# Kernel optimization log

Measured on AMD Instinct MI355X. Metric: run time of the kernel, lower is better.

Reference implementation:

```python
import jax, jax.numpy as jnp
import numpy as np


def _unpack_i4(packed):
    """Unpack int8 bytes into two signed int4 values (low nibble first),
    matching quarot.functional.pack_i4's interleaved layout."""
    p = packed.astype(jnp.int8)
    low = jnp.right_shift(jnp.left_shift(p, 4), 4)   # sign-extended low nibble
    high = jnp.right_shift(p, 4)                      # arithmetic shift -> signed high nibble
    return jnp.stack([low, high], axis=-1).reshape(*p.shape[:-1], p.shape[-1] * 2)


def setup_inputs() -> dict:
    key = jax.random.key(0)
    k1, k2, k3, k4 = jax.random.split(key, 4)
    M, K, N = 4096, 4096, 11008
    # packed int4 activations / weights: each byte holds two signed 4-bit values
    x_q = jax.random.randint(k1, (M, K // 2), 0, 256, dtype=jnp.int32)
    weight = jax.random.randint(k3, (N, K // 2), 0, 256, dtype=jnp.int32)
    # per-row dequant scales (small positive values, as real quant scales are)
    scales_x = (jax.random.uniform(k2, (M, 1), dtype=jnp.float32) * 0.01 + 1e-3).astype(jnp.float16)
    weight_scales = (jax.random.uniform(k4, (N,), dtype=jnp.float32) * 0.01 + 1e-3).astype(jnp.float16)
    return {"x_q": x_q, "scales_x": scales_x, "weight": weight, "weight_scales": weight_scales}


def reference(x_q, scales_x, weight, weight_scales):
    # Unpack int4 -> exact small integers; fp32 matmul accumulates them exactly
    # (|sum| <= 8*8*4096 < 2^24), emulating quarot.fuse_matmul's int4 GEMM.
    A = _unpack_i4(x_q).astype(jnp.float32)      # [M, K]
    B = _unpack_i4(weight).astype(jnp.float32)   # [N, K]
    acc = jnp.einsum('mk,nk->mn', A, B)          # [M, N] integer-exact GEMM
    # fused per-row (activation) x per-channel (weight) dequantization
    out = acc * scales_x.astype(jnp.float32) * weight_scales.astype(jnp.float32)[None, :]
    return out.astype(jnp.float16)
```

## Files before the change

### kernel.cpp

```cpp
#include <hip/hip_runtime.h>

typedef int v4i __attribute__((ext_vector_type(4)));

#define M_DIM 4096
#define N_DIM 11008
#define K_DIM 4096
#define KP    (K_DIM / 2)
#define NKT   (K_DIM / 64)

__device__ __forceinline__ unsigned pack2(int p) {
    int lo = (p << 28) >> 28;
    int hi = (p << 24) >> 28;
    return (unsigned)(lo & 0xFF) | ((unsigned)(hi & 0xFF) << 8);
}

__device__ __forceinline__ void unpack_group(int4 p, unsigned &slo, unsigned &shi) {
    unsigned c = ((unsigned)p.x & 0xFFu)
               | (((unsigned)p.y & 0xFFu) << 8)
               | (((unsigned)p.z & 0xFFu) << 16)
               | (((unsigned)p.w & 0xFFu) << 24);
    slo = (c & 0x0F0F0F0Fu) | ((c & 0x08080808u) * 30u);
    unsigned d = c >> 4;
    shi = (d & 0x0F0F0F0Fu) | ((d & 0x08080808u) * 30u);
}

__global__ __launch_bounds__(256) void unpack_i4_all(
    const int* __restrict__ inA, const int* __restrict__ inB,
    uint2* __restrict__ out, int n4A, int n4tot)
{
    for (int idx = blockIdx.x * blockDim.x + threadIdx.x; idx < n4tot;
         idx += gridDim.x * blockDim.x) {
        int4 v;
        if (idx < n4A) v = ((const int4*)inA)[idx];
        else           v = ((const int4*)inB)[idx - n4A];
        unsigned d0 = pack2(v.x) | (pack2(v.y) << 16);
        unsigned d1 = pack2(v.z) | (pack2(v.w) << 16);
        out[idx] = make_uint2(d0, d1);
    }
}

__global__ __launch_bounds__(512, 2) void gemm_i8_kernel(
    const unsigned char* __restrict__ A8, const unsigned char* __restrict__ B8,
    const float* __restrict__ sx, const float* __restrict__ sw,
    float* __restrict__ out)
{
    __shared__ v4i smem[8192];
    unsigned char* smemAll = (unsigned char*)smem;

    const int t    = threadIdx.x;
    const int lane = t & 63;
    const int w    = t >> 6;
    const int wm   = w >> 2;
    const int wn   = w & 3;

    const int orig = blockIdx.x;
    const int wgid = (orig & 7) * 86 + (orig >> 3);
    const int bx   = wgid >> 4;
    const int by   = wgid & 15;
    const int rowBase = by * 256;
    const int colBase = bx * 256;

    const int cA0 = t, cA1 = t + 512;
    const int rA0 = (cA0 >> 6) * 16 + (cA0 & 15);
    const int rA1 = (cA1 >> 6) * 16 + (cA1 & 15);
    const int qA0 = ((cA0 >> 4) & 3) * 16;
    const int qA1 = ((cA1 >> 4) & 3) * 16;

    const unsigned char* gA0 = A8 + (size_t)(rowBase + rA0) * K_DIM + qA0;
    const unsigned char* gA1 = A8 + (size_t)(rowBase + rA1) * K_DIM + qA1;
    const unsigned char* gB0 = B8 + (size_t)(colBase + rA0) * K_DIM + qA0;
    const unsigned char* gB1 = B8 + (size_t)(colBase + rA1) * K_DIM + qA1;

    const int oA0 = cA0 * 16;
    const int oA1 = cA1 * 16;
    const int oB0 = 16384 + cA0 * 16;
    const int oB1 = 16384 + cA1 * 16;

    v4i acc[8][4] = {};

#define STAGE_A(S) do {                                                        \
    unsigned char* _sb = smemAll + (((S) & 3) << 15);                          \
    const int _kb = (S) * 64;                                                  \
    __builtin_amdgcn_global_load_lds(                                          \
        (const __attribute__((address_space(1))) void*)(gA0 + _kb),            \
        (__attribute__((address_space(3))) void*)(_sb + oA0), 16, 0, 0);       \
    __builtin_amdgcn_global_load_lds(                                          \
        (const __attribute__((address_space(1))) void*)(gA1 + _kb),            \
        (__attribute__((address_space(3))) void*)(_sb + oA1), 16, 0, 0);       \
} while (0)

#define STAGE_B(S) do {                                                        \
    unsigned char* _sb = smemAll + (((S) & 3) << 15);                          \
    const int _kb = (S) * 64;                                                  \
    __builtin_amdgcn_global_load_lds(                                          \
        (const __attribute__((address_space(1))) void*)(gB0 + _kb),            \
        (__attribute__((address_space(3))) void*)(_sb + oB0), 16, 0, 0);       \
    __builtin_amdgcn_global_load_lds(                                          \
        (const __attribute__((address_space(1))) void*)(gB1 + _kb),            \
        (__attribute__((address_space(3))) void*)(_sb + oB1), 16, 0, 0);       \
} while (0)

#define COMPUTE_PHASED(S, DO_STAGE, SS) do {                                   \
    const unsigned char* _b = smemAll + (((S) & 3) << 15);                     \
    v4i bf[4], af0[4], af1[4];                                                 \
     \
    _Pragma("unroll")                                                          \
    for (int nt = 0; nt < 4; ++nt)                                             \
        bf[nt] = *((const v4i*)(_b + 16384 + (((wn * 4 + nt) * 64 + lane) << 4))); \
    _Pragma("unroll")                                                          \
    for (int mt = 0; mt < 4; ++mt)                                             \
        af0[mt] = *((const v4i*)(_b + (((wm * 8 + mt) * 64 + lane) << 4)));    \
    if (DO_STAGE) STAGE_A(SS);                                                 \
    __builtin_amdgcn_s_barrier();                                              \
    asm volatile("s_waitcnt lgkmcnt(0)" ::: "memory");                         \
    __builtin_amdgcn_sched_barrier(0);                                         \
    __builtin_amdgcn_s_setprio(1);                                             \
    _Pragma("unroll")                                                          \
    for (int mt = 0; mt < 4; ++mt)                                             \
        _Pragma("unroll")                                                      \
        for (int nt = 0; nt < 4; ++nt)                                         \
            acc[mt][nt] = __builtin_amdgcn_mfma_i32_16x16x64_i8(               \
                af0[mt], bf[nt], acc[mt][nt], 0, 0, 0);                        \
    __builtin_amdgcn_s_setprio(0);                                             \
    __builtin_amdgcn_s_barrier();                                              \
    __builtin_amdgcn_sched_barrier(0);                                         \
     \
    _Pragma("unroll")                                                          \
    for (int mt = 0; mt < 4; ++mt)                                             \
        af1[mt] = *((const v4i*)(_b + (((wm * 8 + 4 + mt) * 64 + lane) << 4))); \
    if (DO_STAGE) STAGE_B(SS);                                                 \
    __builtin_amdgcn_s_barrier();                                              \
    asm volatile("s_waitcnt lgkmcnt(0)" ::: "memory");                         \
    __builtin_amdgcn_sched_barrier(0);                                         \
    __builtin_amdgcn_s_setprio(1);                                             \
    _Pragma("unroll")                                                          \
    for (int mt = 0; mt < 4; ++mt)                                             \
        _Pragma("unroll")                                                      \
        for (int nt = 0; nt < 4; ++nt)                                         \
            acc[4 + mt][nt] = __builtin_amdgcn_mfma_i32_16x16x64_i8(           \
                af1[mt], bf[nt], acc[4 + mt][nt], 0, 0, 0);                    \
    __builtin_amdgcn_s_setprio(0);                                             \
} while (0)

    STAGE_A(0); STAGE_B(0);
    STAGE_A(1); STAGE_B(1);
    STAGE_A(2); STAGE_B(2);

    for (int kt = 0; kt < NKT - 3; ++kt) {
        asm volatile("s_waitcnt vmcnt(8)" ::: "memory");
        __builtin_amdgcn_s_barrier();
        __builtin_amdgcn_sched_barrier(0);
        COMPUTE_PHASED(kt, 1, kt + 3);
    }
    asm volatile("s_waitcnt vmcnt(8)" ::: "memory");
    __builtin_amdgcn_s_barrier();
    __builtin_amdgcn_sched_barrier(0);
    COMPUTE_PHASED(NKT - 3, 0, 0);
    asm volatile("s_waitcnt vmcnt(4)" ::: "memory");
    __builtin_amdgcn_s_barrier();
    __builtin_amdgcn_sched_barrier(0);
    COMPUTE_PHASED(NKT - 2, 0, 0);
    asm volatile("s_waitcnt vmcnt(0)" ::: "memory");
    __builtin_amdgcn_s_barrier();
    __builtin_amdgcn_sched_barrier(0);
    COMPUTE_PHASED(NKT - 1, 0, 0);

#undef STAGE_A
#undef STAGE_B
#undef COMPUTE_PHASED

    const int ccol = lane & 15;
    const int crow = (lane >> 4) * 4;

    float xs[8][4];
    #pragma unroll
    for (int mt = 0; mt < 8; ++mt)
        #pragma unroll
        for (int r = 0; r < 4; ++r)
            xs[mt][r] = sx[rowBase + wm * 128 + mt * 16 + crow + r];

    #pragma unroll
    for (int nt = 0; nt < 4; ++nt) {
        const int gn = colBase + wn * 64 + nt * 16 + ccol;
        const float wsc = sw[gn];
        #pragma unroll
        for (int mt = 0; mt < 8; ++mt) {
            const int gm = rowBase + wm * 128 + mt * 16 + crow;
            #pragma unroll
            for (int r = 0; r < 4; ++r) {
                float v = (float)acc[mt][nt][r] * xs[mt][r] * wsc;
                out[(size_t)(gm + r) * N_DIM + gn] = v;
            }
        }
    }
}

__global__ __launch_bounds__(256) void gemm_i4_fused_kernel(
    const int* __restrict__ Aq, const int* __restrict__ Bq,
    const float* __restrict__ sx, const float* __restrict__ sw,
    float* __restrict__ out)
{
    __shared__ v4i smem[1024];
    unsigned char* smemA = (unsigned char*)smem;
    unsigned char* smemB = smemA + 8192;

    const int t    = threadIdx.x;
    const int lane = t & 63;
    const int w    = t >> 6;
    const int wm   = w >> 1;
    const int wn   = w & 1;
    const int rowBase = blockIdx.y * 128;
    const int colBase = blockIdx.x * 128;

    const int c0 = t, c1 = t + 256;
    const int r0 = (c0 >> 6) * 16 + (c0 & 15);
    const int r1 = (c1 >> 6) * 16 + (c1 & 15);
    const int q0 = (c0 >> 4) & 3;
    const int q1 = (c1 >> 4) & 3;

    const int* gA0 = Aq + (size_t)(rowBase + r0) * KP + q0 * 8;
    const int* gA1 = Aq + (size_t)(rowBase + r1) * KP + q1 * 8;
    const int* gB0 = Bq + (size_t)(colBase + r0) * KP + q0 * 8;
    const int* gB1 = Bq + (size_t)(colBase + r1) * KP + q1 * 8;

    v4i* lA0 = (v4i*)(smemA + c0 * 16);
    v4i* lA1 = (v4i*)(smemA + c1 * 16);
    v4i* lB0 = (v4i*)(smemB + c0 * 16);
    v4i* lB1 = (v4i*)(smemB + c1 * 16);

    v4i acc[4][4] = {};

    for (int kb = 0; kb < K_DIM; kb += 64) {
        const int kp = kb >> 1;
        int4 a00 = *(const int4*)(gA0 + kp);
        int4 a01 = *(const int4*)(gA0 + kp + 4);
        int4 a10 = *(const int4*)(gA1 + kp);
        int4 a11 = *(const int4*)(gA1 + kp + 4);
        int4 b00 = *(const int4*)(gB0 + kp);
        int4 b01 = *(const int4*)(gB0 + kp + 4);
        int4 b10 = *(const int4*)(gB1 + kp);
        int4 b11 = *(const int4*)(gB1 + kp + 4);

        __syncthreads();

        unsigned u0, u1, u2, u3;
        unpack_group(a00, u0, u1); unpack_group(a01, u2, u3);
        *lA0 = (v4i){(int)u0, (int)u1, (int)u2, (int)u3};
        unpack_group(a10, u0, u1); unpack_group(a11, u2, u3);
        *lA1 = (v4i){(int)u0, (int)u1, (int)u2, (int)u3};
        unpack_group(b00, u0, u1); unpack_group(b01, u2, u3);
        *lB0 = (v4i){(int)u0, (int)u1, (int)u2, (int)u3};
        unpack_group(b10, u0, u1); unpack_group(b11, u2, u3);
        *lB1 = (v4i){(int)u0, (int)u1, (int)u2, (int)u3};

        __syncthreads();

        v4i af[4], bf[4];
        #pragma unroll
        for (int mt = 0; mt < 4; ++mt)
            af[mt] = *((const v4i*)(smemA + ((wm * 4 + mt) * 64 + lane) * 16));
        #pragma unroll
        for (int nt = 0; nt < 4; ++nt)
            bf[nt] = *((const v4i*)(smemB + ((wn * 4 + nt) * 64 + lane) * 16));

        #pragma unroll
        for (int mt = 0; mt < 4; ++mt)
            #pragma unroll
            for (int nt = 0; nt < 4; ++nt)
                acc[mt][nt] = __builtin_amdgcn_mfma_i32_16x16x64_i8(
                    af[mt], bf[nt], acc[mt][nt], 0, 0, 0);
    }

    const int ccol = lane & 15;
    const int crow = (lane >> 4) * 4;

    float xs[4][4];
    #pragma unroll
    for (int mt = 0; mt < 4; ++mt)
        #pragma unroll
        for (int r = 0; r < 4; ++r)
            xs[mt][r] = sx[rowBase + wm * 64 + mt * 16 + crow + r];

    #pragma unroll
    for (int nt = 0; nt < 4; ++nt) {
        const int gn = colBase + wn * 64 + nt * 16 + ccol;
        const float wsc = sw[gn];
        #pragma unroll
        for (int mt = 0; mt < 4; ++mt) {
            const int gm = rowBase + wm * 64 + mt * 16 + crow;
            #pragma unroll
            for (int r = 0; r < 4; ++r) {
                float v = (float)acc[mt][nt][r] * xs[mt][r] * wsc;
                out[(size_t)(gm + r) * N_DIM + gn] = v;
            }
        }
    }
}

extern "C" void kernel_launch(void* const* d_in, const int* in_sizes, int n_in,
                              void* d_out, int out_size, void* d_ws, size_t ws_size,
                              hipStream_t stream) {
    (void)in_sizes; (void)n_in; (void)out_size;
    const int*   x_q = (const int*)d_in[0];
    const float* sx  = (const float*)d_in[1];
    const int*   w_q = (const int*)d_in[2];
    const float* sw  = (const float*)d_in[3];
    float*       out = (float*)d_out;

    const size_t needA = (size_t)M_DIM * K_DIM;
    const size_t needB = (size_t)N_DIM * K_DIM;
    if (ws_size >= needA + needB) {
        unsigned char* A8 = (unsigned char*)d_ws;
        unsigned char* B8 = A8 + needA;
        const int n4A = M_DIM * KP / 4;
        const int n4B = N_DIM * KP / 4;
        const int n4T = n4A + n4B;
        unpack_i4_all<<<2048, 256, 0, stream>>>(x_q, w_q, (uint2*)d_ws, n4A, n4T);
        gemm_i8_kernel<<<688, 512, 0, stream>>>(A8, B8, sx, sw, out);
    } else {
        dim3 grid(N_DIM / 128, M_DIM / 128);
        gemm_i4_fused_kernel<<<grid, 256, 0, stream>>>(x_q, w_q, sx, sw, out);
    }
}
```

Baseline: 484.1 us.

## Double-buffer register fragments so LDS reads overlap MFMAs of previous k-tile

Replaces the two-phase per-k-tile compute, which had barriers between the A halves, with a software-pipelined loop. Each iteration issues inline-asm ds_read_b128 loads for the next tile's A/B fragments into one register set while the MFMAs run on the other set, and it uses a single barrier per iteration. Staging of A and B global->LDS loads is merged into one macro. This removes the extra barrier and LDS read latency on the critical path, at the cost of doubling fragment registers (24 extra v4i), which may hurt occupancy or cause spills. Wait counts and buffer reuse with a 4-slot ring must remain correct.

After: 491.1 us. About the same (+1.5%).

```diff
diff --git a/kernel.cpp b/kernel.cpp
--- a/kernel.cpp
+++ b/kernel.cpp
@@ -76,9 +76,15 @@
     const int oB0 = 16384 + cA0 * 16;
     const int oB1 = 16384 + cA1 * 16;
 
+    const unsigned ldsBase =
+        (unsigned)(size_t)(__attribute__((address_space(3))) void*)smemAll;
+    const unsigned aAddrBase = ldsBase + (unsigned)(wm * 8192 + lane * 16);
+    const unsigned bAddrBase = ldsBase + (unsigned)(16384 + wn * 4096 + lane * 16);
+
     v4i acc[8][4] = {};
-
-#define STAGE_A(S) do {                                                        \
+    v4i aFA[8], bFA[4], aFB[8], bFB[4];
+
+#define STAGE_AB(S) do {                                                       \
     unsigned char* _sb = smemAll + (((S) & 3) << 15);                          \
     const int _kb = (S) * 64;                                                  \
     __builtin_amdgcn_global_load_lds(                                          \
@@ -87,11 +93,6 @@
     __builtin_amdgcn_global_load_lds(                                          \
         (const __attribute__((address_space(1))) void*)(gA1 + _kb),            \
         (__attribute__((address_space(3))) void*)(_sb + oA1), 16, 0, 0);       \
-} while (0)
-
-#define STAGE_B(S) do {                                                        \
-    unsigned char* _sb = smemAll + (((S) & 3) << 15);                          \
-    const int _kb = (S) * 64;                                                  \
     __builtin_amdgcn_global_load_lds(                                          \
         (const __attribute__((address_space(1))) void*)(gB0 + _kb),            \
         (__attribute__((address_space(3))) void*)(_sb + oB0), 16, 0, 0);       \
@@ -100,74 +101,67 @@
         (__attribute__((address_space(3))) void*)(_sb + oB1), 16, 0, 0);       \
 } while (0)
 
-#define COMPUTE_PHASED(S, DO_STAGE, SS) do {                                   \
-    const unsigned char* _b = smemAll + (((S) & 3) << 15);                     \
-    v4i bf[4], af0[4], af1[4];                                                 \
-     \
-    _Pragma("unroll")                                                          \
-    for (int nt = 0; nt < 4; ++nt)                                             \
-        bf[nt] = *((const v4i*)(_b + 16384 + (((wn * 4 + nt) * 64 + lane) << 4))); \
-    _Pragma("unroll")                                                          \
-    for (int mt = 0; mt < 4; ++mt)                                             \
-        af0[mt] = *((const v4i*)(_b + (((wm * 8 + mt) * 64 + lane) << 4)));    \
-    if (DO_STAGE) STAGE_A(SS);                                                 \
-    __builtin_amdgcn_s_barrier();                                              \
-    asm volatile("s_waitcnt lgkmcnt(0)" ::: "memory");                         \
-    __builtin_amdgcn_sched_barrier(0);                                         \
+#define READ_FRAGS(AS, BS, KT) do {                                            \
+    const unsigned _bo = ((unsigned)(KT) & 3u) << 15;                          \
+    unsigned _aAddr = aAddrBase + _bo;                                         \
+    unsigned _bAddr = bAddrBase + _bo;                                         \
+    asm volatile("ds_read_b128 %0, %1 offset:0"    : "=v"(BS[0]) : "v"(_bAddr)); \
+    asm volatile("ds_read_b128 %0, %1 offset:1024" : "=v"(BS[1]) : "v"(_bAddr)); \
+    asm volatile("ds_read_b128 %0, %1 offset:2048" : "=v"(BS[2]) : "v"(_bAddr)); \
+    asm volatile("ds_read_b128 %0, %1 offset:3072" : "=v"(BS[3]) : "v"(_bAddr)); \
+    asm volatile("ds_read_b128 %0, %1 offset:0"    : "=v"(AS[0]) : "v"(_aAddr)); \
+    asm volatile("ds_read_b128 %0, %1 offset:1024" : "=v"(AS[1]) : "v"(_aAddr)); \
+    asm volatile("ds_read_b128 %0, %1 offset:2048" : "=v"(AS[2]) : "v"(_aAddr)); \
+    asm volatile("ds_read_b128 %0, %1 offset:3072" : "=v"(AS[3]) : "v"(_aAddr)); \
+    asm volatile("ds_read_b128 %0, %1 offset:4096" : "=v"(AS[4]) : "v"(_aAddr)); \
+    asm volatile("ds_read_b128 %0, %1 offset:5120" : "=v"(AS[5]) : "v"(_aAddr)); \
+    asm volatile("ds_read_b128 %0, %1 offset:6144" : "=v"(AS[6]) : "v"(_aAddr)); \
+    asm volatile("ds_read_b128 %0, %1 offset:7168" : "=v"(AS[7]) : "v"(_aAddr)); \
+} while (0)
+
+#define MFMA_ALL(AS, BS) do {                                                  \
     __builtin_amdgcn_s_setprio(1);                                             \
     _Pragma("unroll")                                                          \
-    for (int mt = 0; mt < 4; ++mt)                                             \
+    for (int mt = 0; mt < 8; ++mt)                                             \
         _Pragma("unroll")                                                      \
         for (int nt = 0; nt < 4; ++nt)                                         \
             acc[mt][nt] = __builtin_amdgcn_mfma_i32_16x16x64_i8(               \
-                af0[mt], bf[nt], acc[mt][nt], 0, 0, 0);                        \
-    __builtin_amdgcn_s_setprio(0);                                             \
-    __builtin_amdgcn_s_barrier();                                              \
-    __builtin_amdgcn_sched_barrier(0);                                         \
-     \
-    _Pragma("unroll")                                                          \
-    for (int mt = 0; mt < 4; ++mt)                                             \
-        af1[mt] = *((const v4i*)(_b + (((wm * 8 + 4 + mt) * 64 + lane) << 4))); \
-    if (DO_STAGE) STAGE_B(SS);                                                 \
-    __builtin_amdgcn_s_barrier();                                              \
-    asm volatile("s_waitcnt lgkmcnt(0)" ::: "memory");                         \
-    __builtin_amdgcn_sched_barrier(0);                                         \
-    __builtin_amdgcn_s_setprio(1);                                             \
-    _Pragma("unroll")                                                          \
-    for (int mt = 0; mt < 4; ++mt)                                             \
-        _Pragma("unroll")                                                      \
-        for (int nt = 0; nt < 4; ++nt)                                         \
-            acc[4 + mt][nt] = __builtin_amdgcn_mfma_i32_16x16x64_i8(           \
-                af1[mt], bf[nt], acc[4 + mt][nt], 0, 0, 0);                    \
+                AS[mt], BS[nt], acc[mt][nt], 0, 0, 0);                         \
     __builtin_amdgcn_s_setprio(0);                                             \
 } while (0)
 
-    STAGE_A(0); STAGE_B(0);
-    STAGE_A(1); STAGE_B(1);
-    STAGE_A(2); STAGE_B(2);
-
-    for (int kt = 0; kt < NKT - 3; ++kt) {
-        asm volatile("s_waitcnt vmcnt(8)" ::: "memory");
-        __builtin_amdgcn_s_barrier();
-        __builtin_amdgcn_sched_barrier(0);
-        COMPUTE_PHASED(kt, 1, kt + 3);
-    }
+#define KITER(RA, RB, MA, MB, KT, VMC, DO_STAGE) do {                          \
+    asm volatile("s_waitcnt vmcnt(" #VMC ") lgkmcnt(0)" ::: "memory");         \
+    __builtin_amdgcn_sched_barrier(0);                                         \
+    __builtin_amdgcn_s_barrier();                                              \
+    READ_FRAGS(RA, RB, KT);                                                    \
+    if (DO_STAGE) STAGE_AB((KT) + 3);                                          \
+    __builtin_amdgcn_sched_barrier(0);                                         \
+    MFMA_ALL(MA, MB);                                                          \
+} while (0)
+
+    STAGE_AB(0); STAGE_AB(1); STAGE_AB(2);
     asm volatile("s_waitcnt vmcnt(8)" ::: "memory");
     __builtin_amdgcn_s_barrier();
+    READ_FRAGS(aFA, bFA, 0);
+    STAGE_AB(3);
     __builtin_amdgcn_sched_barrier(0);
-    COMPUTE_PHASED(NKT - 3, 0, 0);
-    asm volatile("s_waitcnt vmcnt(4)" ::: "memory");
-    __builtin_amdgcn_s_barrier();
+
+    for (int kt = 1; kt <= 59; kt += 2) {
+        KITER(aFB, bFB, aFA, bFA, kt,     8, 1);
+        KITER(aFA, bFA, aFB, bFB, kt + 1, 8, 1);
+    }
+    KITER(aFB, bFB, aFA, bFA, 61, 8, 0);
+    KITER(aFA, bFA, aFB, bFB, 62, 4, 0);
+    KITER(aFB, bFB, aFA, bFA, 63, 0, 0);
+    asm volatile("s_waitcnt lgkmcnt(0)" ::: "memory");
     __builtin_amdgcn_sched_barrier(0);
-    COMPUTE_PHASED(NKT - 2, 0, 0);
-    asm volatile("s_waitcnt vmcnt(0)" ::: "memory");
-    __builtin_amdgcn_s_barrier();
-    __builtin_amdgcn_sched_barrier(0);
-    COMPUTE_PHASED(NKT - 1, 0, 0);
-
-#undef STAGE_A
-#undef STAGE_B
-#undef COMPUTE_PHASED
+    MFMA_ALL(aFB, bFB);
+
+#undef STAGE_AB
+#undef READ_FRAGS
+#undef MFMA_ALL
+#undef KITER
 
     const int ccol = lane & 15;
     const int crow = (lane >> 4) * 4;
```

## Keep operands as packed int4 in workspace and unpack in registers before MFMA

Applied to the files above, without the earlier changes.

The preprocessing pass now packs the int32-per-byte inputs into dense int4 bytes instead of expanding them to int8, halving its output size and the workspace. The GEMM stages packed tiles covering K=128 into LDS and sign-extends nibbles in registers into two int8 fragments per load, then issues two i8 MFMAs per fragment pair. This halves global and LDS traffic per K step and cuts the barrier count per tile by dropping the two-phase A/B staging. In exchange it adds VALU unpack work inside the MFMA loop, which could compete with matrix issue and raise register pressure.

New measurement: 497.1 us. +2.7%, slower.

```diff
diff --git a/kernel.cpp b/kernel.cpp
--- a/kernel.cpp
+++ b/kernel.cpp
@@ -6,7 +6,8 @@
 #define N_DIM 11008
 #define K_DIM 4096
 #define KP    (K_DIM / 2)
-#define NKT   (K_DIM / 64)
+#define KPB   (K_DIM / 2)
+#define NKT2  (K_DIM / 128)
 
 __device__ __forceinline__ unsigned pack2(int p) {
     int lo = (p << 28) >> 28;
@@ -24,23 +25,37 @@
     shi = (d & 0x0F0F0F0Fu) | ((d & 0x08080808u) * 30u);
 }
 
-__global__ __launch_bounds__(256) void unpack_i4_all(
+__device__ __forceinline__ int sx4(unsigned u) {
+    unsigned a = u & 0x0F0F0F0Fu;
+    unsigned s = u & 0x08080808u;
+    return (int)(a | ((s << 5) - (s << 1)));
+}
+
+__device__ __forceinline__ void unpack16(v4i r, v4i &f0, v4i &f1) {
+    unsigned w0 = (unsigned)r[0], w1 = (unsigned)r[1];
+    unsigned w2 = (unsigned)r[2], w3 = (unsigned)r[3];
+    f0[0] = sx4(w0); f0[1] = sx4(w0 >> 4); f0[2] = sx4(w1); f0[3] = sx4(w1 >> 4);
+    f1[0] = sx4(w2); f1[1] = sx4(w2 >> 4); f1[2] = sx4(w3); f1[3] = sx4(w3 >> 4);
+}
+
+__global__ __launch_bounds__(256) void pack_i4_all(
     const int* __restrict__ inA, const int* __restrict__ inB,
-    uint2* __restrict__ out, int n4A, int n4tot)
+    unsigned* __restrict__ out, int n4A, int n4tot)
 {
     for (int idx = blockIdx.x * blockDim.x + threadIdx.x; idx < n4tot;
          idx += gridDim.x * blockDim.x) {
         int4 v;
         if (idx < n4A) v = ((const int4*)inA)[idx];
         else           v = ((const int4*)inB)[idx - n4A];
-        unsigned d0 = pack2(v.x) | (pack2(v.y) << 16);
-        unsigned d1 = pack2(v.z) | (pack2(v.w) << 16);
-        out[idx] = make_uint2(d0, d1);
-    }
-}
-
-__global__ __launch_bounds__(512, 2) void gemm_i8_kernel(
-    const unsigned char* __restrict__ A8, const unsigned char* __restrict__ B8,
+        out[idx] = ((unsigned)v.x & 0xFFu)
+                 | (((unsigned)v.y & 0xFFu) << 8)
+                 | (((unsigned)v.z & 0xFFu) << 16)
+                 | (((unsigned)v.w & 0xFFu) << 24);
+    }
+}
+
+__global__ __launch_bounds__(512, 2) void gemm_i4p_kernel(
+    const unsigned char* __restrict__ A4, const unsigned char* __restrict__ B4,
     const float* __restrict__ sx, const float* __restrict__ sw,
     float* __restrict__ out)
 {
@@ -66,10 +81,10 @@
     const int qA0 = ((cA0 >> 4) & 3) * 16;
     const int qA1 = ((cA1 >> 4) & 3) * 16;
 
-    const unsigned char* gA0 = A8 + (size_t)(rowBase + rA0) * K_DIM + qA0;
-    const unsigned char* gA1 = A8 + (size_t)(rowBase + rA1) * K_DIM + qA1;
-    const unsigned char* gB0 = B8 + (size_t)(colBase + rA0) * K_DIM + qA0;
-    const unsigned char* gB1 = B8 + (size_t)(colBase + rA1) * K_DIM + qA1;
+    const unsigned char* gA0 = A4 + (size_t)(rowBase + rA0) * KPB + qA0;
+    const unsigned char* gA1 = A4 + (size_t)(rowBase + rA1) * KPB + qA1;
+    const unsigned char* gB0 = B4 + (size_t)(colBase + rA0) * KPB + qA0;
+    const unsigned char* gB1 = B4 + (size_t)(colBase + rA1) * KPB + qA1;
 
     const int oA0 = cA0 * 16;
     const int oA1 = cA1 * 16;
@@ -78,7 +93,7 @@
 
     v4i acc[8][4] = {};
 
-#define STAGE_A(S) do {                                                        \
+#define STAGE_AB(S) do {                                                       \
     unsigned char* _sb = smemAll + (((S) & 3) << 15);                          \
     const int _kb = (S) * 64;                                                  \
     __builtin_amdgcn_global_load_lds(                                          \
@@ -87,11 +102,6 @@
     __builtin_amdgcn_global_load_lds(                                          \
         (const __attribute__((address_space(1))) void*)(gA1 + _kb),            \
         (__attribute__((address_space(3))) void*)(_sb + oA1), 16, 0, 0);       \
-} while (0)
-
-#define STAGE_B(S) do {                                                        \
-    unsigned char* _sb = smemAll + (((S) & 3) << 15);                          \
-    const int _kb = (S) * 64;                                                  \
     __builtin_amdgcn_global_load_lds(                                          \
         (const __attribute__((address_space(1))) void*)(gB0 + _kb),            \
         (__attribute__((address_space(3))) void*)(_sb + oB0), 16, 0, 0);       \
@@ -100,74 +110,58 @@
         (__attribute__((address_space(3))) void*)(_sb + oB1), 16, 0, 0);       \
 } while (0)
 
-#define COMPUTE_PHASED(S, DO_STAGE, SS) do {                                   \
-    const unsigned char* _b = smemAll + (((S) & 3) << 15);                     \
-    v4i bf[4], af0[4], af1[4];                                                 \
-     \
+#define TILE(KT, DO_STAGE) do {                                                \
+    const unsigned char* _b = smemAll + (((KT) & 3) << 15);                    \
+    v4i braw[4], araw[8];                                                      \
     _Pragma("unroll")                                                          \
     for (int nt = 0; nt < 4; ++nt)                                             \
-        bf[nt] = *((const v4i*)(_b + 16384 + (((wn * 4 + nt) * 64 + lane) << 4))); \
+        braw[nt] = *((const v4i*)(_b + 16384 + (((wn * 4 + nt) * 64 + lane) << 4))); \
     _Pragma("unroll")                                                          \
-    for (int mt = 0; mt < 4; ++mt)                                             \
-        af0[mt] = *((const v4i*)(_b + (((wm * 8 + mt) * 64 + lane) << 4)));    \
-    if (DO_STAGE) STAGE_A(SS);                                                 \
-    __builtin_amdgcn_s_barrier();                                              \
-    asm volatile("s_waitcnt lgkmcnt(0)" ::: "memory");                         \
-    __builtin_amdgcn_sched_barrier(0);                                         \
-    __builtin_amdgcn_s_setprio(1);                                             \
+    for (int mt = 0; mt < 8; ++mt)                                             \
+        araw[mt] = *((const v4i*)(_b + (((wm * 8 + mt) * 64 + lane) << 4)));   \
+    if (DO_STAGE) STAGE_AB((KT) + 3);                                          \
+    v4i bf0[4], bf1[4];                                                        \
     _Pragma("unroll")                                                          \
-    for (int mt = 0; mt < 4; ++mt)                                             \
+    for (int nt = 0; nt < 4; ++nt) unpack16(braw[nt], bf0[nt], bf1[nt]);       \
+    _Pragma("unroll")                                                          \
+    for (int mt = 0; mt < 8; ++mt) {                                           \
+        v4i a0, a1;                                                            \
+        unpack16(araw[mt], a0, a1);                                            \
+        __builtin_amdgcn_s_setprio(1);                                         \
         _Pragma("unroll")                                                      \
-        for (int nt = 0; nt < 4; ++nt)                                         \
+        for (int nt = 0; nt < 4; ++nt) {                                       \
             acc[mt][nt] = __builtin_amdgcn_mfma_i32_16x16x64_i8(               \
-                af0[mt], bf[nt], acc[mt][nt], 0, 0, 0);                        \
-    __builtin_amdgcn_s_setprio(0);                                             \
-    __builtin_amdgcn_s_barrier();                                              \
-    __builtin_amdgcn_sched_barrier(0);                                         \
-     \
-    _Pragma("unroll")                                                          \
-    for (int mt = 0; mt < 4; ++mt)                                             \
-        af1[mt] = *((const v4i*)(_b + (((wm * 8 + 4 + mt) * 64 + lane) << 4))); \
-    if (DO_STAGE) STAGE_B(SS);                                                 \
-    __builtin_amdgcn_s_barrier();                                              \
-    asm volatile("s_waitcnt lgkmcnt(0)" ::: "memory");                         \
-    __builtin_amdgcn_sched_barrier(0);                                         \
-    __builtin_amdgcn_s_setprio(1);                                             \
-    _Pragma("unroll")                                                          \
-    for (int mt = 0; mt < 4; ++mt)                                             \
-        _Pragma("unroll")                                                      \
-        for (int nt = 0; nt < 4; ++nt)                                         \
-            acc[4 + mt][nt] = __builtin_amdgcn_mfma_i32_16x16x64_i8(           \
-                af1[mt], bf[nt], acc[4 + mt][nt], 0, 0, 0);                    \
-    __builtin_amdgcn_s_setprio(0);                                             \
+                a0, bf0[nt], acc[mt][nt], 0, 0, 0);                            \
+            acc[mt][nt] = __builtin_amdgcn_mfma_i32_16x16x64_i8(               \
+                a1, bf1[nt], acc[mt][nt], 0, 0, 0);                            \
+        }                                                                      \
+        __builtin_amdgcn_s_setprio(0);                                         \
+    }                                                                          \
 } while (0)
 
-    STAGE_A(0); STAGE_B(0);
-    STAGE_A(1); STAGE_B(1);
-    STAGE_A(2); STAGE_B(2);
-
-    for (int kt = 0; kt < NKT - 3; ++kt) {
+    STAGE_AB(0); STAGE_AB(1); STAGE_AB(2);
+
+    for (int kt = 0; kt < NKT2 - 3; ++kt) {
         asm volatile("s_waitcnt vmcnt(8)" ::: "memory");
         __builtin_amdgcn_s_barrier();
         __builtin_amdgcn_sched_barrier(0);
-        COMPUTE_PHASED(kt, 1, kt + 3);
+        TILE(kt, 1);
     }
     asm volatile("s_waitcnt vmcnt(8)" ::: "memory");
     __builtin_amdgcn_s_barrier();
     __builtin_amdgcn_sched_barrier(0);
-    COMPUTE_PHASED(NKT - 3, 0, 0);
+    TILE(NKT2 - 3, 0);
     asm volatile("s_waitcnt vmcnt(4)" ::: "memory");
     __builtin_amdgcn_s_barrier();
     __builtin_amdgcn_sched_barrier(0);
-    COMPUTE_PHASED(NKT - 2, 0, 0);
+    TILE(NKT2 - 2, 0);
     asm volatile("s_waitcnt vmcnt(0)" ::: "memory");
     __builtin_amdgcn_s_barrier();
     __builtin_amdgcn_sched_barrier(0);
-    COMPUTE_PHASED(NKT - 1, 0, 0);
-
-#undef STAGE_A
-#undef STAGE_B
-#undef COMPUTE_PHASED
+    TILE(NKT2 - 1, 0);
+
+#undef STAGE_AB
+#undef TILE
 
     const int ccol = lane & 15;
     const int crow = (lane >> 4) * 4;
@@ -307,16 +301,16 @@
     const float* sw  = (const float*)d_in[3];
     float*       out = (float*)d_out;
 
-    const size_t needA = (size_t)M_DIM * K_DIM;
-    const size_t needB = (size_t)N_DIM * K_DIM;
+    const size_t needA = (size_t)M_DIM * KPB;
+    const size_t needB = (size_t)N_DIM * KPB;
     if (ws_size >= needA + needB) {
-        unsigned char* A8 = (unsigned char*)d_ws;
-        unsigned char* B8 = A8 + needA;
+        unsigned char* A4 = (unsigned char*)d_ws;
+        unsigned char* B4 = A4 + needA;
         const int n4A = M_DIM * KP / 4;
         const int n4B = N_DIM * KP / 4;
         const int n4T = n4A + n4B;
-        unpack_i4_all<<<2048, 256, 0, stream>>>(x_q, w_q, (uint2*)d_ws, n4A, n4T);
-        gemm_i8_kernel<<<688, 512, 0, stream>>>(A8, B8, sx, sw, out);
+        pack_i4_all<<<2048, 256, 0, stream>>>(x_q, w_q, (unsigned*)d_ws, n4A, n4T);
+        gemm_i4p_kernel<<<688, 512, 0, stream>>>(A4, B4, sx, sw, out);
     } else {
         dim3 grid(N_DIM / 128, M_DIM / 128);
         gemm_i4_fused_kernel<<<grid, 256, 0, stream>>>(x_q, w_q, sx, sw, out);
```
